# Kernel optimization log

Measured on AMD Instinct MI355X. Metric: run time of the kernel, lower is better.

The kernel has to match this reference:

```python
import jax, jax.numpy as jnp
import numpy as np

B, L, D = 4, 4096, 1024


def setup_inputs() -> dict:
    key = jax.random.key(0)
    ks = jax.random.split(key, 10)
    s = 1.0 / np.sqrt(D)  # torch Linear default init scale
    return {
        "x": jax.random.normal(ks[0], (B, L, D), dtype=jnp.float32),
        "hidden": jax.random.normal(ks[1], (B, D), dtype=jnp.float32),
        "W_ln_z": jax.random.uniform(ks[2], (D, D), jnp.float32, -s, s),
        "b_ln_z": jax.random.uniform(ks[3], (D,), jnp.float32, -s, s),
        "W_dt": jax.random.uniform(ks[4], (D, D), jnp.float32, -s, s),
        "b_dt": jax.random.uniform(ks[5], (D,), jnp.float32, -s, s),
        "W_y": jax.random.uniform(ks[6], (D, D), jnp.float32, -s, s),
        "b_y": jax.random.uniform(ks[7], (D,), jnp.float32, -s, s),
        "W_g": jax.random.uniform(ks[8], (D, D), jnp.float32, -s, s),
        "b_g": jax.random.uniform(ks[9], (D,), jnp.float32, -s, s),
    }


def reference(x, hidden, W_ln_z, b_ln_z, W_dt, b_dt, W_y, b_y, W_g, b_g):
    # Linear projections (torch Linear: x @ W.T + b)
    z_pre = x @ W_ln_z.T + b_ln_z          # (B, L, D)
    dt_pre = x @ W_dt.T + b_dt             # (B, L, D)

    # -softplus(-u) == log_sigmoid(u)
    ln_z = jax.nn.log_sigmoid(z_pre)       # ln z
    ln_da = jax.nn.log_sigmoid(dt_pre)     # ln(delta*a)
    ln_z_da = ln_z + ln_da
    ln_o_da = jax.nn.log_sigmoid(-dt_pre)  # -softplus(dt_pre)

    ln_o_da_cumsum = jnp.cumsum(ln_o_da, axis=1)
    # log-space parallel scan: h_t = sum_{s<=t} z_s*da_s * prod_{s<r<=t} o_da_r
    lcse = jax.lax.cumlogsumexp(ln_z_da - ln_o_da_cumsum, axis=1)
    h_inner = jnp.exp(lcse + ln_o_da_cumsum)                       # (B, L, D)
    h_cross = jnp.exp(ln_o_da_cumsum) * hidden[:, None, :]         # (B, L, D)
    h = h_inner + h_cross

    gate = jax.nn.silu(x @ W_g.T + b_g)
    y = (h @ W_y.T + b_y) * gate
    return y, h
```

## Files before the change

kernel.cpp:

```cpp
#include <hip/hip_runtime.h>


#define BDIM 4
#define LDIM 4096
#define DDIM 1024
#define MROWS (BDIM * LDIM)
#define KDIM 1024
#define NPROJ 3072
#define NCHUNK 64
#define LCHUNK 64

typedef __attribute__((ext_vector_type(8))) short short8v;
typedef __attribute__((ext_vector_type(4))) float f32x4;

__device__ __forceinline__ float bf2f(short u) {
    union { float f; unsigned int i; } v;
    v.i = ((unsigned int)(unsigned short)u) << 16;
    return v.f;
}
__device__ __forceinline__ short f2bf(float f) {
    union { float f; unsigned int i; } v; v.f = f;
    unsigned int r = v.i + 0x7FFFu + ((v.i >> 16) & 1u);
    return (short)(r >> 16);
}
__device__ __forceinline__ float sigf(float x) { return 1.f / (1.f + __expf(-x)); }

__global__ void cast_f32_bf16(const float* __restrict__ src, short* __restrict__ dst, int n4) {
    int i = blockIdx.x * blockDim.x + threadIdx.x;
    int stride = gridDim.x * blockDim.x;
    for (; i < n4; i += stride) {
        float4 v = reinterpret_cast<const float4*>(src)[i];
        short4 o;
        o.x = f2bf(v.x); o.y = f2bf(v.y); o.z = f2bf(v.z); o.w = f2bf(v.w);
        reinterpret_cast<short4*>(dst)[i] = o;
    }
}

__global__ void cast4_f32_bf16(const float* __restrict__ s0, const float* __restrict__ s1,
                               const float* __restrict__ s2, const float* __restrict__ s3,
                               short* __restrict__ dst) {
    int i = blockIdx.x * blockDim.x + threadIdx.x;
    int seg = i >> 18, off = i & ((1 << 18) - 1);
    const float* s = (seg == 0) ? s0 : (seg == 1) ? s1 : (seg == 2) ? s2 : s3;
    float4 v = reinterpret_cast<const float4*>(s)[off];
    short4 o;
    o.x = f2bf(v.x); o.y = f2bf(v.y); o.z = f2bf(v.z); o.w = f2bf(v.w);
    reinterpret_cast<short4*>(dst)[i] = o;
}


#define STAGE(arr, gbase, half, kofs)                                              \
  do {                                                                             \
    _Pragma("unroll")                                                              \
    for (int _i = 0; _i < 2; ++_i) {                                               \
      int _c = _i * 512 + tid;                                                     \
      int _row = _c >> 3, _g = _c & 7;                                             \
      int _gsw = _g ^ (_row & 7);                                                  \
      __builtin_amdgcn_global_load_lds(                                            \
        (const __attribute__((address_space(1))) void*)(                           \
            (gbase) + (size_t)((half) * 128 + _row) * K + (kofs) + _gsw * 8),      \
        (__attribute__((address_space(3))) void*)(                                 \
            &arr[(_i * 512 + wid * 64) * 8]),                                      \
        16, 0, 0);                                                                 \
    }                                                                              \
  } while (0)

#define LDA4(dst, arr)                                                             \
  _Pragma("unroll")                                                                \
  for (int _m = 0; _m < 4; ++_m) {                                                 \
    int _r = _m * 32 + wm * 16 + lrow;                                             \
    _Pragma("unroll")                                                              \
    for (int _kk = 0; _kk < 2; ++_kk)                                              \
      dst[_m][_kk] = *(const short8v*)&arr[_r * 64 +                               \
                       (((_kk * 4 + kq) ^ (lrow & 7)) * 8)];                       \
  }

#define LDB2(dst, arr)                                                             \
  _Pragma("unroll")                                                                \
  for (int _n = 0; _n < 2; ++_n) {                                                 \
    int _r = _n * 64 + wn * 16 + lrow;                                             \
    _Pragma("unroll")                                                              \
    for (int _kk = 0; _kk < 2; ++_kk)                                              \
      dst[_n][_kk] = *(const short8v*)&arr[_r * 64 +                               \
                       (((_kk * 4 + kq) ^ (lrow & 7)) * 8)];                       \
  }

#define MFMAQ(mi0, ni0, afr, bfr)                                                  \
  __builtin_amdgcn_s_setprio(1);                                                   \
  _Pragma("unroll")                                                                \
  for (int _kk = 0; _kk < 2; ++_kk)                                                \
    _Pragma("unroll")                                                              \
    for (int _m = 0; _m < 4; ++_m)                                                 \
      _Pragma("unroll")                                                            \
      for (int _n = 0; _n < 2; ++_n)                                               \
        acc[(mi0) + _m][(ni0) + _n] = __builtin_amdgcn_mfma_f32_16x16x32_bf16(     \
            afr[_m][_kk], bfr[_n][_kk], acc[(mi0) + _m][(ni0) + _n], 0, 0, 0);     \
  __builtin_amdgcn_s_setprio(0);

#define BARB()   __builtin_amdgcn_s_barrier()
#define VM4()    asm volatile("s_waitcnt vmcnt(4)")
#define VM0()    asm volatile("s_waitcnt vmcnt(0)")

template<int OUT_BF16, int HAS_GATE>
__global__ __launch_bounds__(512, 2) void gemm256(
    const short* __restrict__ A, const short* __restrict__ Bm,
    const float* __restrict__ bias, void* __restrict__ Cv,
    int M, int N, int K,
    const short* __restrict__ gate, int ldg)
{
    __shared__ short As0h0[8192], As0h1[8192], As1h0[8192], As1h1[8192];
    __shared__ short Bs0h0[8192], Bs0h1[8192], Bs1h0[8192], Bs1h1[8192];

    const int tid  = threadIdx.x;
    const int lane = tid & 63;
    const int wid  = tid >> 6;
    const int wm   = wid >> 2;
    const int wn   = wid & 3;
    const int lrow = lane & 15;
    const int kq   = lane >> 4;

    const int gx  = gridDim.x;
    const int nwg = gx * gridDim.y;
    int flat = blockIdx.y * gx + blockIdx.x;
    if ((nwg & 7) == 0) { int q = nwg >> 3; flat = (flat & 7) * q + (flat >> 3); }
    const int m0 = (flat / gx) * 256;
    const int n0 = (flat % gx) * 256;

    const short* Abase = A + (size_t)m0 * K;
    const short* Bbase = Bm + (size_t)n0 * K;

    f32x4 acc[8][4];
#pragma unroll
    for (int i = 0; i < 8; ++i)
#pragma unroll
        for (int j = 0; j < 4; ++j)
            acc[i][j] = (f32x4){0.f, 0.f, 0.f, 0.f};

    STAGE(As0h0, Abase, 0, 0);
    STAGE(As0h1, Abase, 1, 0);
    STAGE(Bs0h0, Bbase, 0, 0);
    STAGE(Bs0h1, Bbase, 1, 0);
    STAGE(As1h0, Abase, 0, 64);
    STAGE(Bs1h0, Bbase, 0, 64);
    VM4(); BARB();

    const int NT = K / 64;
    for (int t = 0; t < NT; t += 2) {
        const int k1 = (t + 1) * 64, k2 = (t + 2) * 64, k3 = (t + 3) * 64;
        const bool more = (t + 2) < NT;
        short8v af[4][2], b0[2][2], b1[2][2];

        LDA4(af, As0h0) LDB2(b0, Bs0h0)
        STAGE(As1h1, Abase, 1, k1);
        BARB(); MFMAQ(0, 0, af, b0)

        LDB2(b1, Bs0h1)
        STAGE(Bs1h1, Bbase, 1, k1);
        BARB(); MFMAQ(0, 2, af, b1)

        LDA4(af, As0h1)
        if (more) STAGE(As0h0, Abase, 0, k2);
        BARB(); MFMAQ(4, 2, af, b1)

        if (more) { STAGE(Bs0h0, Bbase, 0, k2); VM4(); } else { VM0(); }
        BARB(); MFMAQ(4, 0, af, b0)

        LDA4(af, As1h0) LDB2(b0, Bs1h0)
        if (more) STAGE(As0h1, Abase, 1, k2);
        BARB(); MFMAQ(0, 0, af, b0)

        LDB2(b1, Bs1h1)
        if (more) STAGE(Bs0h1, Bbase, 1, k2);
        BARB(); MFMAQ(0, 2, af, b1)

        LDA4(af, As1h1)
        if (more) STAGE(As1h0, Abase, 0, k3);
        BARB(); MFMAQ(4, 2, af, b1)

        if (more) { STAGE(Bs1h0, Bbase, 0, k3); VM4(); }
        BARB(); MFMAQ(4, 0, af, b0)
    }

    const int lr4 = (lane >> 4) * 4;
#pragma unroll
    for (int mi = 0; mi < 8; ++mi) {
        int rowb = m0 + mi * 32 + wm * 16 + lr4;
#pragma unroll
        for (int ni = 0; ni < 4; ++ni) {
            int col = n0 + ni * 64 + wn * 16 + lrow;
            float bv = bias[col];
#pragma unroll
            for (int r = 0; r < 4; ++r) {
                int row = rowb + r;
                float val = acc[mi][ni][r] + bv;
                if (HAS_GATE) {
                    float g = bf2f(gate[(size_t)row * ldg + col]);
                    val *= g * sigf(g);
                }
                if (OUT_BF16)
                    ((short*)Cv)[(size_t)row * N + col] = f2bf(val);
                else
                    ((float*)Cv)[(size_t)row * N + col] = val;
            }
        }
    }
}

__global__ __launch_bounds__(512) void chunk_reduce(
    const short* __restrict__ pre, float* __restrict__ sA, float* __restrict__ sBv)
{
    const int t = threadIdx.x;
    const int c = blockIdx.x;
    const int b = blockIdx.y;
    float A0 = 1.f, A1 = 1.f, B0 = 0.f, B1 = 0.f;
    size_t base = ((size_t)(b * LDIM) + c * LCHUNK) * NPROJ;
    for (int i = 0; i < LCHUNK; ++i) {
        unsigned int zz = *reinterpret_cast<const unsigned int*>(&pre[base + 2 * t]);
        unsigned int dd = *reinterpret_cast<const unsigned int*>(&pre[base + DDIM + 2 * t]);
        float z0 = bf2f((short)(zz & 0xffff)), z1 = bf2f((short)(zz >> 16));
        float d0 = bf2f((short)(dd & 0xffff)), d1 = bf2f((short)(dd >> 16));
        float e0 = __expf(-d0), r0 = 1.f / (1.f + e0), o0 = e0 * r0, q0 = sigf(z0) * r0;
        float e1 = __expf(-d1), r1 = 1.f / (1.f + e1), o1 = e1 * r1, q1 = sigf(z1) * r1;
        B0 = q0 + o0 * B0; A0 *= o0;
        B1 = q1 + o1 * B1; A1 *= o1;
        base += NPROJ;
    }
    int idx = ((b * NCHUNK + c) << 10) + 2 * t;
    *reinterpret_cast<float2*>(&sA[idx])  = make_float2(A0, A1);
    *reinterpret_cast<float2*>(&sBv[idx]) = make_float2(B0, B1);
}

__global__ __launch_bounds__(1024) void chunk_prefix(
    const float* __restrict__ sA, const float* __restrict__ sBv,
    const float* __restrict__ hidden, float* __restrict__ sI)
{
    const int d = threadIdx.x;
    const int b = blockIdx.x;
    float h = hidden[b * DDIM + d];
    for (int c = 0; c < NCHUNK; ++c) {
        int idx = ((b * NCHUNK + c) << 10) + d;
        sI[idx] = h;
        h = sBv[idx] + sA[idx] * h;
    }
}

__global__ __launch_bounds__(512) void chunk_apply(
    const short* __restrict__ pre, const float* __restrict__ sI,
    float* __restrict__ hout, short* __restrict__ hbf)
{
    const int t = threadIdx.x;
    const int c = blockIdx.x;
    const int b = blockIdx.y;
    float2 hi = *reinterpret_cast<const float2*>(&sI[((b * NCHUNK + c) << 10) + 2 * t]);
    float h0 = hi.x, h1 = hi.y;
    size_t base  = ((size_t)(b * LDIM) + c * LCHUNK) * NPROJ;
    size_t obase = ((size_t)(b * LDIM) + c * LCHUNK) * DDIM + 2 * t;
    for (int i = 0; i < LCHUNK; ++i) {
        unsigned int zz = *reinterpret_cast<const unsigned int*>(&pre[base + 2 * t]);
        unsigned int dd = *reinterpret_cast<const unsigned int*>(&pre[base + DDIM + 2 * t]);
        float z0 = bf2f((short)(zz & 0xffff)), z1 = bf2f((short)(zz >> 16));
        float d0 = bf2f((short)(dd & 0xffff)), d1 = bf2f((short)(dd >> 16));
        float e0 = __expf(-d0), r0 = 1.f / (1.f + e0), o0 = e0 * r0, q0 = sigf(z0) * r0;
        float e1 = __expf(-d1), r1 = 1.f / (1.f + e1), o1 = e1 * r1, q1 = sigf(z1) * r1;
        h0 = q0 + o0 * h0;
        h1 = q1 + o1 * h1;
        *reinterpret_cast<float2*>(&hout[obase]) = make_float2(h0, h1);
        unsigned int hp = ((unsigned int)(unsigned short)f2bf(h0)) |
                          (((unsigned int)(unsigned short)f2bf(h1)) << 16);
        *reinterpret_cast<unsigned int*>(&hbf[obase]) = hp;
        base += NPROJ;
        obase += DDIM;
    }
}

extern "C" void kernel_launch(void* const* d_in, const int* in_sizes, int n_in,
                              void* d_out, int out_size, void* d_ws, size_t ws_size,
                              hipStream_t stream) {
    const float* x      = (const float*)d_in[0];
    const float* hidden = (const float*)d_in[1];
    const float* W_ln_z = (const float*)d_in[2];
    const float* b_ln_z = (const float*)d_in[3];
    const float* W_dt   = (const float*)d_in[4];
    const float* b_dt   = (const float*)d_in[5];
    const float* W_y    = (const float*)d_in[6];
    const float* b_y    = (const float*)d_in[7];
    const float* W_g    = (const float*)d_in[8];
    const float* b_g    = (const float*)d_in[9];

    char* ws = (char*)d_ws;
    short* x_bf   = (short*)(ws + 0);
    short* Wcat   = (short*)(ws + 33554432);
    short* Wy_bf  = (short*)(ws + 39845888);
    float* biascat= (float*)(ws + 41943040);
    short* pre    = (short*)(ws + 41955328);
    float* sA     = (float*)(ws + 142618624);
    float* sBv    = (float*)(ws + 143667200);
    float* sI     = (float*)(ws + 144715776);

    cast_f32_bf16<<<2048, 256, 0, stream>>>(x, x_bf, (MROWS * KDIM) / 4);
    cast4_f32_bf16<<<4096, 256, 0, stream>>>(W_ln_z, W_dt, W_g, W_y, Wcat);

    hipMemcpyAsync(biascat,            b_ln_z, DDIM * sizeof(float), hipMemcpyDeviceToDevice, stream);
    hipMemcpyAsync(biascat + DDIM,     b_dt,   DDIM * sizeof(float), hipMemcpyDeviceToDevice, stream);
    hipMemcpyAsync(biascat + 2 * DDIM, b_g,    DDIM * sizeof(float), hipMemcpyDeviceToDevice, stream);

    gemm256<1, 0><<<dim3(NPROJ / 256, MROWS / 256), 512, 0, stream>>>(
        x_bf, Wcat, biascat, pre, MROWS, NPROJ, KDIM, nullptr, 0);

    float* y_out = (float*)d_out;
    float* h_out = (float*)d_out + (size_t)MROWS * DDIM;
    short* h_bf  = x_bf;
    chunk_reduce<<<dim3(NCHUNK, BDIM), 512, 0, stream>>>(pre, sA, sBv);
    chunk_prefix<<<dim3(BDIM), 1024, 0, stream>>>(sA, sBv, hidden, sI);
    chunk_apply<<<dim3(NCHUNK, BDIM), 512, 0, stream>>>(pre, sI, h_out, h_bf);

    gemm256<0, 1><<<dim3(DDIM / 256, MROWS / 256), 512, 0, stream>>>(
        h_bf, Wy_bf, b_y, y_out, MROWS, DDIM, KDIM, pre + 2 * DDIM, NPROJ);
}
```

Measured before the change: 264.8 us.

## Replace eight-phase half-tile GEMM pipeline with simple double buffering

Replaces the fine-grained ping-pong schedule, which had eight barriers per two k-tiles and kept several half-tile loads in flight, with plain double buffering. Each iteration now issues all four stage loads for the next tile, computes on the current buffer, then waits with vmcnt(0) and a barrier. Scheduling barriers keep the compiler from mixing the loads into the MFMA stream. This cuts barrier count and simplifies the code, but each tile now drains all outstanding loads before the next, which may expose memory latency.

```diff
diff --git a/kernel.cpp b/kernel.cpp
--- a/kernel.cpp
+++ b/kernel.cpp
@@ -98,8 +98,8 @@
   __builtin_amdgcn_s_setprio(0);
 
 #define BARB()   __builtin_amdgcn_s_barrier()
-#define VM4()    asm volatile("s_waitcnt vmcnt(4)")
 #define VM0()    asm volatile("s_waitcnt vmcnt(0)")
+#define SCHEDB() __builtin_amdgcn_sched_barrier(0)
 
 template<int OUT_BF16, int HAS_GATE>
 __global__ __launch_bounds__(512, 2) void gemm256(
@@ -140,45 +140,33 @@
     STAGE(As0h1, Abase, 1, 0);
     STAGE(Bs0h0, Bbase, 0, 0);
     STAGE(Bs0h1, Bbase, 1, 0);
-    STAGE(As1h0, Abase, 0, 64);
-    STAGE(Bs1h0, Bbase, 0, 64);
-    VM4(); BARB();
+    VM0(); BARB();
 
     const int NT = K / 64;
     for (int t = 0; t < NT; t += 2) {
-        const int k1 = (t + 1) * 64, k2 = (t + 2) * 64, k3 = (t + 3) * 64;
+        const int k1 = (t + 1) * 64, k2 = (t + 2) * 64;
         const bool more = (t + 2) < NT;
         short8v af[4][2], b0[2][2], b1[2][2];
 
-        LDA4(af, As0h0) LDB2(b0, Bs0h0)
-        STAGE(As1h1, Abase, 1, k1);
-        BARB(); MFMAQ(0, 0, af, b0)
-
-        LDB2(b1, Bs0h1)
-        STAGE(Bs1h1, Bbase, 1, k1);
-        BARB(); MFMAQ(0, 2, af, b1)
-
+        STAGE(As1h0, Abase, 0, k1); STAGE(As1h1, Abase, 1, k1);
+        STAGE(Bs1h0, Bbase, 0, k1); STAGE(Bs1h1, Bbase, 1, k1);
+        SCHEDB();
+        LDA4(af, As0h0) LDB2(b0, Bs0h0) LDB2(b1, Bs0h1)
+        MFMAQ(0, 0, af, b0) MFMAQ(0, 2, af, b1)
         LDA4(af, As0h1)
-        if (more) STAGE(As0h0, Abase, 0, k2);
-        BARB(); MFMAQ(4, 2, af, b1)
-
-        if (more) { STAGE(Bs0h0, Bbase, 0, k2); VM4(); } else { VM0(); }
-        BARB(); MFMAQ(4, 0, af, b0)
-
-        LDA4(af, As1h0) LDB2(b0, Bs1h0)
-        if (more) STAGE(As0h1, Abase, 1, k2);
-        BARB(); MFMAQ(0, 0, af, b0)
-
-        LDB2(b1, Bs1h1)
-        if (more) STAGE(Bs0h1, Bbase, 1, k2);
-        BARB(); MFMAQ(0, 2, af, b1)
-
+        MFMAQ(4, 2, af, b1) MFMAQ(4, 0, af, b0)
+        VM0(); BARB();
+
+        if (more) {
+            STAGE(As0h0, Abase, 0, k2); STAGE(As0h1, Abase, 1, k2);
+            STAGE(Bs0h0, Bbase, 0, k2); STAGE(Bs0h1, Bbase, 1, k2);
+        }
+        SCHEDB();
+        LDA4(af, As1h0) LDB2(b0, Bs1h0) LDB2(b1, Bs1h1)
+        MFMAQ(0, 0, af, b0) MFMAQ(0, 2, af, b1)
         LDA4(af, As1h1)
-        if (more) STAGE(As1h0, Abase, 0, k3);
-        BARB(); MFMAQ(4, 2, af, b1)
-
-        if (more) { STAGE(Bs1h0, Bbase, 0, k3); VM4(); }
-        BARB(); MFMAQ(4, 0, af, b0)
+        MFMAQ(4, 2, af, b1) MFMAQ(4, 0, af, b0)
+        VM0(); BARB();
     }
 
     const int lr4 = (lane >> 4) * 4;
```

Result: slower. 283.4 us (+7.0%).
